# Optimization experiments

Measured on AMD Instinct MI355X. Metric: run time of the kernel, lower is better.

Reference implementation:

```python
import jax, jax.numpy as jnp
import numpy as np

V = 32000      # vocab_size
E = 256        # ModelConfig.n_embed
T_BLOCK = 2048 # ModelConfig.block_size
H = 4          # n_head (hardcoded in Bigram)
L = 3          # number of Blocks
HS = E // H    # head_size
EPS = 1e-5

def _ln(x, g, b):
    mu = jnp.mean(x, axis=-1, keepdims=True)
    var = jnp.var(x, axis=-1, keepdims=True)
    return (x - mu) * jax.lax.rsqrt(var + EPS) * g + b

def setup_inputs() -> dict:
    key = jax.random.key(0)
    ks = jax.random.split(key, 16)
    s = 0.02
    inp = {
        "idx": jax.random.randint(ks[0], (4, T_BLOCK), 0, V),
        "tok_emb": jax.random.normal(ks[1], (V, E), jnp.float32) * s,
        "pos_emb": jax.random.normal(ks[2], (T_BLOCK, E), jnp.float32) * s,
        # per-layer stacked params (heads concatenated -> full ExE projections)
        "Wq": jax.random.normal(ks[3], (L, E, E), jnp.float32) * s,
        "Wk": jax.random.normal(ks[4], (L, E, E), jnp.float32) * s,
        "Wv": jax.random.normal(ks[5], (L, E, E), jnp.float32) * s,
        "Wproj": jax.random.normal(ks[6], (L, E, E), jnp.float32) * s,
        "bproj": jnp.zeros((L, E), jnp.float32),
        "ln1_g": jnp.ones((L, E), jnp.float32),
        "ln1_b": jnp.zeros((L, E), jnp.float32),
        "W1": jax.random.normal(ks[7], (L, E, 4 * E), jnp.float32) * s,
        "b1": jnp.zeros((L, 4 * E), jnp.float32),
        "W2": jax.random.normal(ks[8], (L, 4 * E, E), jnp.float32) * s,
        "b2": jnp.zeros((L, E), jnp.float32),
        "ln2_g": jnp.ones((L, E), jnp.float32),
        "ln2_b": jnp.zeros((L, E), jnp.float32),
        "Wlm": jax.random.normal(ks[9], (E, V), jnp.float32) * s,
        "blm": jnp.zeros((V,), jnp.float32),
    }
    return inp

def reference(idx, tok_emb, pos_emb, Wq, Wk, Wv, Wproj, bproj, ln1_g, ln1_b,
              W1, b1, W2, b2, ln2_g, ln2_b, Wlm, blm):
    B, T = idx.shape
    x = tok_emb[idx] + pos_emb[:T]  # [B,T,E]
    causal = jnp.tril(jnp.ones((T, T), bool))
    # NOTE: source scales by C**0.5 with C = n_embed (not head_size)
    scale = 1.0 / jnp.sqrt(jnp.float32(E))
    for l in range(L):
        h = _ln(x, ln1_g[l], ln1_b[l])
        q = (h @ Wq[l]).reshape(B, T, H, HS).transpose(0, 2, 1, 3)
        k = (h @ Wk[l]).reshape(B, T, H, HS).transpose(0, 2, 1, 3)
        v = (h @ Wv[l]).reshape(B, T, H, HS).transpose(0, 2, 1, 3)
        wei = jnp.einsum('bhtd,bhsd->bhts', q, k) * scale
        wei = jnp.where(causal, wei, -jnp.inf)
        wei = jax.nn.softmax(wei, axis=-1)
        y = jnp.einsum('bhts,bhsd->bhtd', wei, v)
        y = y.transpose(0, 2, 1, 3).reshape(B, T, E)
        x = x + y @ Wproj[l] + bproj[l]
        h2 = _ln(x, ln2_g[l], ln2_b[l])
        x = x + jax.nn.relu(h2 @ W1[l] + b1[l]) @ W2[l] + b2[l]
    # ln_f exists in __init__ but is never applied in forward — skipped.
    logits = x @ Wlm + blm  # [B,T,V]
    return logits
```

## Files before the change

### kernel.cpp

```cpp
#include <hip/hip_runtime.h>
#include <hip/hip_bf16.h>

#define EMB 256
#define NHEAD 4
#define HSZ 64
#define NLAYER 3
#define TBLK 2048
#define VOCAB 32000
#define BATCH 4
#define LNEPS 1e-5f
#define BT (BATCH * TBLK)
#define QKVD (3 * EMB)

typedef __attribute__((ext_vector_type(8))) short bf16x8v;
typedef __attribute__((ext_vector_type(4))) float f32x4;
typedef unsigned short u16;
typedef unsigned int u32;

__device__ __forceinline__ u16 f2bf(float f) {
    union { float f; u32 u; } c; c.f = f;
    u32 r = c.u + 0x7fff + ((c.u >> 16) & 1);
    return (u16)(r >> 16);
}
__device__ __forceinline__ u32 pack2(float a, float b) {
    return (u32)f2bf(a) | ((u32)f2bf(b) << 16);
}

__device__ __forceinline__ void gload16(const u16* g, u16* l) {
    __builtin_amdgcn_global_load_lds(
        (__attribute__((address_space(1))) void*)g,
        (__attribute__((address_space(3))) void*)l, 16, 0, 0);
}

__global__ __launch_bounds__(256) void embed_kernel(
    const int* __restrict__ idx, const float* __restrict__ tok,
    const float* __restrict__ pos, float* __restrict__ x)
{
    const int row = blockIdx.x * 4 + (threadIdx.x >> 6);
    const int t = row & (TBLK - 1);
    const int token = idx[row];
    const int e = (threadIdx.x & 63) * 4;
    const float4 tv = *(const float4*)&tok[(size_t)token * EMB + e];
    const float4 pv = *(const float4*)&pos[(size_t)t * EMB + e];
    float4 o;
    o.x = tv.x + pv.x; o.y = tv.y + pv.y; o.z = tv.z + pv.z; o.w = tv.w + pv.w;
    *(float4*)&x[(size_t)row * EMB + e] = o;
}

__global__ __launch_bounds__(256) void ln_kernel(
    const float* __restrict__ x, const float* __restrict__ g,
    const float* __restrict__ b, u16* __restrict__ out)
{
    const int row = blockIdx.x * 4 + (threadIdx.x >> 6);
    const int e = (threadIdx.x & 63) * 4;
    const float4 xv = *(const float4*)&x[(size_t)row * EMB + e];
    float s1 = xv.x + xv.y + xv.z + xv.w;
    float s2 = xv.x * xv.x + xv.y * xv.y + xv.z * xv.z + xv.w * xv.w;
    #pragma unroll
    for (int off = 32; off >= 1; off >>= 1) {
        s1 += __shfl_xor(s1, off);
        s2 += __shfl_xor(s2, off);
    }
    const float mu  = s1 * (1.0f / EMB);
    const float var = s2 * (1.0f / EMB) - mu * mu;
    const float rs  = rsqrtf(var + LNEPS);
    const float4 gv = *(const float4*)&g[e];
    const float4 bv = *(const float4*)&b[e];
    ushort4 o;
    o.x = f2bf((xv.x - mu) * rs * gv.x + bv.x);
    o.y = f2bf((xv.y - mu) * rs * gv.y + bv.y);
    o.z = f2bf((xv.z - mu) * rs * gv.z + bv.z);
    o.w = f2bf((xv.w - mu) * rs * gv.w + bv.w);
    *(ushort4*)&out[(size_t)row * EMB + e] = o;
}

__global__ __launch_bounds__(256) void transpose_cast(
    const float* __restrict__ W, u16* __restrict__ Wt, int K, int N,
    size_t sW, size_t sWt)
{
    __shared__ float t[32][33];
    W  += (size_t)blockIdx.z * sW;
    Wt += (size_t)blockIdx.z * sWt;
    const int bx = blockIdx.x, by = blockIdx.y;
    const int tx = threadIdx.x, ty = threadIdx.y;
    #pragma unroll
    for (int i = 0; i < 32; i += 8)
        t[ty + i][tx] = W[(size_t)(by * 32 + ty + i) * N + bx * 32 + tx];
    __syncthreads();
    #pragma unroll
    for (int i = 0; i < 32; i += 8)
        Wt[(size_t)(bx * 32 + ty + i) * K + by * 32 + tx] = f2bf(t[tx][ty + i]);
}

__global__ __launch_bounds__(256) void transpose_qkvp(
    const float* __restrict__ Wq, const float* __restrict__ Wk,
    const float* __restrict__ Wv, const float* __restrict__ Wp,
    u16* __restrict__ Wqkvt, u16* __restrict__ Wprojt)
{
    __shared__ float t[32][33];
    const int which = blockIdx.z & 3, l = blockIdx.z >> 2;
    const float* W;
    u16* Wt;
    switch (which) {
        case 0: W = Wq + (size_t)l*EMB*EMB; Wt = Wqkvt + (size_t)l*QKVD*EMB;               break;
        case 1: W = Wk + (size_t)l*EMB*EMB; Wt = Wqkvt + (size_t)l*QKVD*EMB + EMB*EMB;     break;
        case 2: W = Wv + (size_t)l*EMB*EMB; Wt = Wqkvt + (size_t)l*QKVD*EMB + 2*EMB*EMB;   break;
        default:W = Wp + (size_t)l*EMB*EMB; Wt = Wprojt + (size_t)l*EMB*EMB;               break;
    }
    const int bx = blockIdx.x, by = blockIdx.y;
    const int tx = threadIdx.x, ty = threadIdx.y;
    #pragma unroll
    for (int i = 0; i < 32; i += 8)
        t[ty + i][tx] = W[(size_t)(by * 32 + ty + i) * EMB + bx * 32 + tx];
    __syncthreads();
    #pragma unroll
    for (int i = 0; i < 32; i += 8)
        Wt[(size_t)(bx * 32 + ty + i) * EMB + by * 32 + tx] = f2bf(t[tx][ty + i]);
}

template<int BNT, int BIAS, int RES, int RELU, int OUTBF>
__global__ __launch_bounds__(256) void mgemm(
    const u16* __restrict__ A, const u16* __restrict__ Bt,
    const float* __restrict__ bias, const float* __restrict__ res,
    void* __restrict__ Cv, int M, int N, int K)
{
    constexpr int MI = (BNT == 128) ? 4 : 2;
    __shared__ u16 Al[2][128 * 32];
    __shared__ u16 Bl[2][BNT * 32];
    const int tid = threadIdx.x;
    const int bm = blockIdx.x, bn = blockIdx.y;
    const int wid = tid >> 6, lane = tid & 63;
    const int wr = (BNT == 128) ? (wid >> 1) * 64 : wid * 32;
    const int wc = (BNT == 128) ? (wid & 1) * 64 : 0;
    const int fr = lane & 15, fq = lane >> 4;

    const int l4 = lane >> 2;
    const int lc_src = ((lane & 3) ^ ((l4 >> 1) & 3)) * 8;
    const u16* Aga = A  + (size_t)(bm * 128 + wid * 16 + l4) * K + lc_src;
    const u16* Bga = Bt + (size_t)(bn * BNT + wid * 16 + l4) * K + lc_src;
    const int lin = (wid * 16 + l4) * 32 + (lane & 3) * 8;

    const int rsw = (fq ^ ((fr >> 1) & 3)) * 8;

    f32x4 acc[MI][4];
    #pragma unroll
    for (int i = 0; i < MI; ++i)
        #pragma unroll
        for (int j = 0; j < 4; ++j)
            acc[i][j] = f32x4{0.f, 0.f, 0.f, 0.f};

    gload16(Aga,                  &Al[0][lin]);
    gload16(Aga + (size_t)64 * K, &Al[0][lin + 64 * 32]);
    gload16(Bga,                  &Bl[0][lin]);
    if (BNT == 128) gload16(Bga + (size_t)64 * K, &Bl[0][lin + 64 * 32]);

    int buf = 0;
    for (int k0 = 0; k0 < K; k0 += 32, buf ^= 1) {
        __syncthreads();
        if (k0 + 32 < K) {
            gload16(Aga + k0 + 32,                  &Al[buf ^ 1][lin]);
            gload16(Aga + (size_t)64 * K + k0 + 32, &Al[buf ^ 1][lin + 64 * 32]);
            gload16(Bga + k0 + 32,                  &Bl[buf ^ 1][lin]);
            if (BNT == 128)
                gload16(Bga + (size_t)64 * K + k0 + 32, &Bl[buf ^ 1][lin + 64 * 32]);
        }
        bf16x8v af[MI], bfr[4];
        #pragma unroll
        for (int mi = 0; mi < MI; ++mi)
            af[mi] = *(const bf16x8v*)&Al[buf][(wr + mi * 16 + fr) * 32 + rsw];
        #pragma unroll
        for (int ni = 0; ni < 4; ++ni)
            bfr[ni] = *(const bf16x8v*)&Bl[buf][(wc + ni * 16 + fr) * 32 + rsw];
        #pragma unroll
        for (int mi = 0; mi < MI; ++mi)
            #pragma unroll
            for (int ni = 0; ni < 4; ++ni)
                acc[mi][ni] = __builtin_amdgcn_mfma_f32_16x16x32_bf16(
                    af[mi], bfr[ni], acc[mi][ni], 0, 0, 0);
    }

    float* Cf = (float*)Cv;
    u16*   Cb = (u16*)Cv;
    #pragma unroll
    for (int mi = 0; mi < MI; ++mi) {
        #pragma unroll
        for (int j = 0; j < 4; ++j) {
            const int r = bm * 128 + wr + mi * 16 + fq * 4 + j;
            #pragma unroll
            for (int ni = 0; ni < 4; ++ni) {
                const int c = bn * BNT + wc + ni * 16 + fr;
                float v = acc[mi][ni][j];
                if (BIAS) v += bias[c];
                if (RELU) v = fmaxf(v, 0.f);
                if (RES)  v += res[(size_t)r * N + c];
                if (OUTBF) Cb[(size_t)r * N + c] = f2bf(v);
                else       Cf[(size_t)r * N + c] = v;
            }
        }
    }
}

__global__ __launch_bounds__(256) void attn_kernel(
    const u16* __restrict__ qkv, u16* __restrict__ y)
{
    constexpr int LDK = 72;
    __shared__ u16 Kl[2][64 * LDK];
    __shared__ u16 Vt[2][64 * LDK];

    const int tid = threadIdx.x;
    const int qt = (int)gridDim.x - 1 - (int)blockIdx.x;
    const int bh = blockIdx.y;
    const int b = bh >> 2, h = bh & 3;
    const int w = tid >> 6, lane = tid & 63;
    const int fr = lane & 15, fq = lane >> 4;
    const size_t rowbase = (size_t)b * TBLK;
    const int qoff = h * HSZ, koff = EMB + h * HSZ, voff = 2 * EMB + h * HSZ;
    const int qg = qt * 64 + w * 16 + fr;

    bf16x8v qf[2];
    #pragma unroll
    for (int ks = 0; ks < 2; ++ks)
        qf[ks] = *(const bf16x8v*)&qkv[(rowbase + qg) * QKVD + qoff + ks * 32 + fq * 8];

    f32x4 yac[4];
    #pragma unroll
    for (int mi = 0; mi < 4; ++mi) yac[mi] = f32x4{0.f, 0.f, 0.f, 0.f};
    float m = -1e30f, l = 0.f;

    const int skv = tid >> 2, sc = (tid & 3) * 16;
    const u16* kbase = &qkv[(rowbase + skv) * QKVD + koff + sc];
    const u16* vbase = &qkv[(rowbase + skv) * QKVD + voff + sc];

    bf16x8v kr0 = *(const bf16x8v*)kbase;
    bf16x8v kr1 = *(const bf16x8v*)(kbase + 8);
    bf16x8v vr0 = *(const bf16x8v*)vbase;
    bf16x8v vr1 = *(const bf16x8v*)(vbase + 8);

    int buf = 0;
    for (int kv0 = 0; kv0 <= qt * 64; kv0 += 64, buf ^= 1) {
        {
            u16* Kw = &Kl[buf][skv * LDK + sc];
            *(bf16x8v*)Kw = kr0; *(bf16x8v*)(Kw + 8) = kr1;
            #pragma unroll
            for (int i = 0; i < 8; ++i) Vt[buf][(sc + i) * LDK + skv] = (u16)vr0[i];
            #pragma unroll
            for (int i = 0; i < 8; ++i) Vt[buf][(sc + 8 + i) * LDK + skv] = (u16)vr1[i];
        }
        __syncthreads();
        if (kv0 + 64 <= qt * 64) {
            const size_t off = (size_t)(kv0 + 64) * QKVD;
            kr0 = *(const bf16x8v*)(kbase + off);
            kr1 = *(const bf16x8v*)(kbase + off + 8);
            vr0 = *(const bf16x8v*)(vbase + off);
            vr1 = *(const bf16x8v*)(vbase + off + 8);
        }

        f32x4 st[4];
        __builtin_amdgcn_s_setprio(1);
        #pragma unroll
        for (int mb = 0; mb < 4; ++mb) {
            st[mb] = f32x4{0.f, 0.f, 0.f, 0.f};
            #pragma unroll
            for (int ks = 0; ks < 2; ++ks) {
                const bf16x8v kf = *(const bf16x8v*)
                    &Kl[buf][(mb * 16 + fr) * LDK + ks * 32 + fq * 8];
                st[mb] = __builtin_amdgcn_mfma_f32_16x16x32_bf16(
                    kf, qf[ks], st[mb], 0, 0, 0);
            }
        }
        __builtin_amdgcn_s_setprio(0);
        float p[4][4];
        float mloc = -1e30f;
        #pragma unroll
        for (int mb = 0; mb < 4; ++mb)
            #pragma unroll
            for (int j = 0; j < 4; ++j) {
                const int kvg = kv0 + mb * 16 + fq * 4 + j;
                const float s = (kvg <= qg) ? st[mb][j] * 0.0625f : -1e30f;
                p[mb][j] = s;
                mloc = fmaxf(mloc, s);
            }
    mloc = fmaxf(mloc, __shfl_xor(mloc, 16));
        mloc = fmaxf(mloc, __shfl_xor(mloc, 32));
        const float mnew = fmaxf(m, mloc);
        const float alpha = __expf(m - mnew);
        float rsum = 0.f;
        #pragma unroll
        for (int mb = 0; mb < 4; ++mb)
            #pragma unroll
            for (int j = 0; j < 4; ++j) {
                p[mb][j] = __expf(p[mb][j] - mnew);
                rsum += p[mb][j];
            }
        rsum += __shfl_xor(rsum, 16);
        rsum += __shfl_xor(rsum, 32);
        l = l * alpha + rsum;
        m = mnew;
        #pragma unroll
        for (int mi = 0; mi < 4; ++mi) yac[mi] *= alpha;

        u32 pk[4][2];
        #pragma unroll
        for (int mb = 0; mb < 4; ++mb) {
            pk[mb][0] = pack2(p[mb][0], p[mb][1]);
            pk[mb][1] = pack2(p[mb][2], p[mb][3]);
        }
        #pragma unroll
        for (int ksv = 0; ksv < 2; ++ksv) {
            union { u32 u[4]; bf16x8v v; } pf;
            #pragma unroll
            for (int t = 0; t < 4; ++t) {
                const int srcl = ((fq & 1) * 2 + (t >> 1)) * 16 + fr;
                const u32 lo = __shfl(pk[ksv * 2 + 0][t & 1], srcl);
                const u32 hi = __shfl(pk[ksv * 2 + 1][t & 1], srcl);
                pf.u[t] = (fq >> 1) ? hi : lo;
            }
            __builtin_amdgcn_s_setprio(1);
            #pragma unroll
            for (int mi = 0; mi < 4; ++mi) {
                const bf16x8v vf = *(const bf16x8v*)
                    &Vt[buf][(mi * 16 + fr) * LDK + ksv * 32 + fq * 8];
                yac[mi] = __builtin_amdgcn_mfma_f32_16x16x32_bf16(
                    vf, pf.v, yac[mi], 0, 0, 0);
            }
            __builtin_amdgcn_s_setprio(0);
        }
    }

    const float inv = 1.f / l;
    #pragma unroll
    for (int mi = 0; mi < 4; ++mi) {
        ushort4 o;
        o.x = f2bf(yac[mi][0] * inv);
        o.y = f2bf(yac[mi][1] * inv);
        o.z = f2bf(yac[mi][2] * inv);
        o.w = f2bf(yac[mi][3] * inv);
        *(ushort4*)&y[(rowbase + qg) * EMB + h * HSZ + mi * 16 + fq * 4] = o;
    }
}

extern "C" void kernel_launch(void* const* d_in, const int* in_sizes, int n_in,
                              void* d_out, int out_size, void* d_ws, size_t ws_size,
                              hipStream_t stream) {
    const int*   idx   = (const int*)  d_in[0];
    const float* tok   = (const float*)d_in[1];
    const float* pos   = (const float*)d_in[2];
    const float* Wq    = (const float*)d_in[3];
    const float* Wk    = (const float*)d_in[4];
    const float* Wv    = (const float*)d_in[5];
    const float* Wproj = (const float*)d_in[6];
    const float* bproj = (const float*)d_in[7];
    const float* ln1g  = (const float*)d_in[8];
    const float* ln1b  = (const float*)d_in[9];
    const float* W1    = (const float*)d_in[10];
    const float* b1    = (const float*)d_in[11];
    const float* W2    = (const float*)d_in[12];
    const float* b2    = (const float*)d_in[13];
    const float* ln2g  = (const float*)d_in[14];
    const float* ln2b  = (const float*)d_in[15];
    const float* Wlm   = (const float*)d_in[16];
    const float* blm   = (const float*)d_in[17];
    float* out = (float*)d_out;

    float* x    = (float*)d_ws;
    u16*   hb   = (u16*)(x + (size_t)BT * EMB);
    u16*   qkvb = hb + (size_t)BT * EMB;
    u16*   yb   = qkvb + (size_t)BT * QKVD;
    u16*   hid  = qkvb;
    u16*   Wqkvt  = yb + (size_t)BT * EMB;
    u16*   Wprojt = Wqkvt  + (size_t)NLAYER * QKVD * EMB;
    u16*   W1t    = Wprojt + (size_t)NLAYER * EMB * EMB;
    u16*   W2t    = W1t    + (size_t)NLAYER * EMB * 4 * EMB;
    u16*   Wlmt   = W2t    + (size_t)NLAYER * 4 * EMB * EMB;

    const dim3 tb(32, 8);
    transpose_qkvp<<<dim3(8, 8, NLAYER * 4), tb, 0, stream>>>(
        Wq, Wk, Wv, Wproj, Wqkvt, Wprojt);
    transpose_cast<<<dim3(32, 8, NLAYER), tb, 0, stream>>>(
        W1, W1t, EMB, 4*EMB, (size_t)EMB*4*EMB, (size_t)EMB*4*EMB);
    transpose_cast<<<dim3(8, 32, NLAYER), tb, 0, stream>>>(
        W2, W2t, 4*EMB, EMB, (size_t)4*EMB*EMB, (size_t)4*EMB*EMB);
    transpose_cast<<<dim3(VOCAB/32, 8, 1), tb, 0, stream>>>(
        Wlm, Wlmt, EMB, VOCAB, 0, 0);

    embed_kernel<<<BT/4, 256, 0, stream>>>(idx, tok, pos, x);

    for (int l = 0; l < NLAYER; ++l) {
        ln_kernel<<<BT/4, 256, 0, stream>>>(x, ln1g + l*EMB, ln1b + l*EMB, hb);
        mgemm<128,0,0,0,1><<<dim3(BT/128, QKVD/128), 256, 0, stream>>>(
            hb, Wqkvt + (size_t)l*QKVD*EMB, nullptr, nullptr, qkvb, BT, QKVD, EMB);
        attn_kernel<<<dim3(TBLK/64, BATCH*NHEAD), 256, 0, stream>>>(qkvb, yb);
        mgemm<64,1,1,0,0><<<dim3(BT/128, EMB/64), 256, 0, stream>>>(
            yb, Wprojt + (size_t)l*EMB*EMB, bproj + l*EMB, x, x, BT, EMB, EMB);
        ln_kernel<<<BT/4, 256, 0, stream>>>(x, ln2g + l*EMB, ln2b + l*EMB, hb);
        mgemm<128,1,0,1,1><<<dim3(BT/128, 4*EMB/128), 256, 0, stream>>>(
            hb, W1t + (size_t)l*EMB*4*EMB, b1 + l*4*EMB, nullptr, hid, BT, 4*EMB, EMB);
        if (l < NLAYER - 1) {
            mgemm<64,1,1,0,0><<<dim3(BT/128, EMB/64), 256, 0, stream>>>(
                hid, W2t + (size_t)l*4*EMB*EMB, b2 + l*EMB, x, x, BT, EMB, 4*EMB);
        } else {
            mgemm<64,1,1,0,1><<<dim3(BT/128, EMB/64), 256, 0, stream>>>(
                hid, W2t + (size_t)l*4*EMB*EMB, b2 + l*EMB, x, hb, BT, EMB, 4*EMB);
        }
    }

    mgemm<128,1,0,0,0><<<dim3(BT/128, VOCAB/128), 256, 0, stream>>>(
        hb, Wlmt, blm, nullptr, out, BT, VOCAB, EMB);
}
```

Baseline: 690.2 us.

## Restructure GEMM to 64x64 tiles with full 256-wide K chunks in LDS

Replaces the double-buffered 128xBNT tile GEMM (K step 32) with a 64x64 tile that loads a whole 256-wide K chunk of A and B into LDS (64 KB) with an XOR swizzle, then runs 8 MFMA k-steps between barriers. This cuts the number of barriers and gives more blocks to fill the GPU, especially for the N=256 projections. The cost is lower arithmetic intensity per tile, no overlap of loads with compute, and heavy LDS use that limits occupancy. The large LM-head GEMM now launches 4x more blocks with smaller reuse.

```diff
diff --git a/kernel.cpp b/kernel.cpp
--- a/kernel.cpp
+++ b/kernel.cpp
@@ -118,77 +118,76 @@
         Wt[(size_t)(bx * 32 + ty + i) * EMB + by * 32 + tx] = f2bf(t[tx][ty + i]);
 }
 
-template<int BNT, int BIAS, int RES, int RELU, int OUTBF>
+template<int BIAS, int RES, int RELU, int OUTBF>
 __global__ __launch_bounds__(256) void mgemm(
     const u16* __restrict__ A, const u16* __restrict__ Bt,
     const float* __restrict__ bias, const float* __restrict__ res,
     void* __restrict__ Cv, int M, int N, int K)
 {
-    constexpr int MI = (BNT == 128) ? 4 : 2;
-    __shared__ u16 Al[2][128 * 32];
-    __shared__ u16 Bl[2][BNT * 32];
+    __shared__ u16 Al[64 * 256];
+    __shared__ u16 Bl[64 * 256];
     const int tid = threadIdx.x;
     const int bm = blockIdx.x, bn = blockIdx.y;
     const int wid = tid >> 6, lane = tid & 63;
-    const int wr = (BNT == 128) ? (wid >> 1) * 64 : wid * 32;
-    const int wc = (BNT == 128) ? (wid & 1) * 64 : 0;
+    const int wr = (wid >> 1) * 32, wc = (wid & 1) * 32;
     const int fr = lane & 15, fq = lane >> 4;
 
-    const int l4 = lane >> 2;
-    const int lc_src = ((lane & 3) ^ ((l4 >> 1) & 3)) * 8;
-    const u16* Aga = A  + (size_t)(bm * 128 + wid * 16 + l4) * K + lc_src;
-    const u16* Bga = Bt + (size_t)(bn * BNT + wid * 16 + l4) * K + lc_src;
-    const int lin = (wid * 16 + l4) * 32 + (lane & 3) * 8;
-
-    const int rsw = (fq ^ ((fr >> 1) & 3)) * 8;
-
-    f32x4 acc[MI][4];
-    #pragma unroll
-    for (int i = 0; i < MI; ++i)
-        #pragma unroll
-        for (int j = 0; j < 4; ++j)
+    const int srow = tid >> 5;
+    const int sch  = (tid & 31) ^ srow;
+    const u16* Ag = A  + (size_t)(bm * 64 + srow) * K + sch * 8;
+    const u16* Bg = Bt + (size_t)(bn * 64 + srow) * K + sch * 8;
+    const int ldst = tid * 8;
+
+    const int frs = fr & 7;
+
+    f32x4 acc[2][2];
+    #pragma unroll
+    for (int i = 0; i < 2; ++i)
+        #pragma unroll
+        for (int j = 0; j < 2; ++j)
             acc[i][j] = f32x4{0.f, 0.f, 0.f, 0.f};
 
-    gload16(Aga,                  &Al[0][lin]);
-    gload16(Aga + (size_t)64 * K, &Al[0][lin + 64 * 32]);
-    gload16(Bga,                  &Bl[0][lin]);
-    if (BNT == 128) gload16(Bga + (size_t)64 * K, &Bl[0][lin + 64 * 32]);
-
-    int buf = 0;
-    for (int k0 = 0; k0 < K; k0 += 32, buf ^= 1) {
+    const int nc = K >> 8;
+    for (int c = 0; c < nc; ++c) {
+        if (c) __syncthreads();
+        const size_t cofs = (size_t)c << 8;
+        #pragma unroll
+        for (int R = 0; R < 8; ++R)
+            gload16(Ag + cofs + (size_t)R * 8 * K, &Al[R * 2048 + ldst]);
+        #pragma unroll
+        for (int R = 0; R < 8; ++R)
+            gload16(Bg + cofs + (size_t)R * 8 * K, &Bl[R * 2048 + ldst]);
         __syncthreads();
-        if (k0 + 32 < K) {
-            gload16(Aga + k0 + 32,                  &Al[buf ^ 1][lin]);
-            gload16(Aga + (size_t)64 * K + k0 + 32, &Al[buf ^ 1][lin + 64 * 32]);
-            gload16(Bga + k0 + 32,                  &Bl[buf ^ 1][lin]);
-            if (BNT == 128)
-                gload16(Bga + (size_t)64 * K + k0 + 32, &Bl[buf ^ 1][lin + 64 * 32]);
-        }
-        bf16x8v af[MI], bfr[4];
-        #pragma unroll
-        for (int mi = 0; mi < MI; ++mi)
-            af[mi] = *(const bf16x8v*)&Al[buf][(wr + mi * 16 + fr) * 32 + rsw];
-        #pragma unroll
-        for (int ni = 0; ni < 4; ++ni)
-            bfr[ni] = *(const bf16x8v*)&Bl[buf][(wc + ni * 16 + fr) * 32 + rsw];
-        #pragma unroll
-        for (int mi = 0; mi < MI; ++mi)
-            #pragma unroll
-            for (int ni = 0; ni < 4; ++ni)
-                acc[mi][ni] = __builtin_amdgcn_mfma_f32_16x16x32_bf16(
-                    af[mi], bfr[ni], acc[mi][ni], 0, 0, 0);
+
+        #pragma unroll
+        for (int ks = 0; ks < 8; ++ks) {
+            const int s8 = (((ks * 4 + fq) ^ frs)) * 8;
+            bf16x8v af[2], bfv[2];
+            #pragma unroll
+            for (int mi = 0; mi < 2; ++mi)
+                af[mi] = *(const bf16x8v*)&Al[(wr + mi * 16 + fr) * 256 + s8];
+            #pragma unroll
+            for (int ni = 0; ni < 2; ++ni)
+                bfv[ni] = *(const bf16x8v*)&Bl[(wc + ni * 16 + fr) * 256 + s8];
+            #pragma unroll
+            for (int mi = 0; mi < 2; ++mi)
+                #pragma unroll
+                for (int ni = 0; ni < 2; ++ni)
+                    acc[mi][ni] = __builtin_amdgcn_mfma_f32_16x16x32_bf16(
+                        af[mi], bfv[ni], acc[mi][ni], 0, 0, 0);
+        }
     }
 
     float* Cf = (float*)Cv;
     u16*   Cb = (u16*)Cv;
     #pragma unroll
-    for (int mi = 0; mi < MI; ++mi) {
+    for (int mi = 0; mi < 2; ++mi) {
         #pragma unroll
         for (int j = 0; j < 4; ++j) {
-            const int r = bm * 128 + wr + mi * 16 + fq * 4 + j;
-            #pragma unroll
-            for (int ni = 0; ni < 4; ++ni) {
-                const int c = bn * BNT + wc + ni * 16 + fr;
+            const int r = bm * 64 + wr + mi * 16 + fq * 4 + j;
+            #pragma unroll
+            for (int ni = 0; ni < 2; ++ni) {
+                const int c = bn * 64 + wc + ni * 16 + fr;
                 float v = acc[mi][ni][j];
                 if (BIAS) v += bias[c];
                 if (RELU) v = fmaxf(v, 0.f);
@@ -280,7 +279,7 @@
                 p[mb][j] = s;
                 mloc = fmaxf(mloc, s);
             }
-    mloc = fmaxf(mloc, __shfl_xor(mloc, 16));
+        mloc = fmaxf(mloc, __shfl_xor(mloc, 16));
         mloc = fmaxf(mloc, __shfl_xor(mloc, 32));
         const float mnew = fmaxf(m, mloc);
         const float alpha = __expf(m - mnew);
@@ -387,23 +386,23 @@
 
     for (int l = 0; l < NLAYER; ++l) {
         ln_kernel<<<BT/4, 256, 0, stream>>>(x, ln1g + l*EMB, ln1b + l*EMB, hb);
-        mgemm<128,0,0,0,1><<<dim3(BT/128, QKVD/128), 256, 0, stream>>>(
+        mgemm<0,0,0,1><<<dim3(BT/64, QKVD/64), 256, 0, stream>>>(
             hb, Wqkvt + (size_t)l*QKVD*EMB, nullptr, nullptr, qkvb, BT, QKVD, EMB);
         attn_kernel<<<dim3(TBLK/64, BATCH*NHEAD), 256, 0, stream>>>(qkvb, yb);
-        mgemm<64,1,1,0,0><<<dim3(BT/128, EMB/64), 256, 0, stream>>>(
+        mgemm<1,1,0,0><<<dim3(BT/64, EMB/64), 256, 0, stream>>>(
             yb, Wprojt + (size_t)l*EMB*EMB, bproj + l*EMB, x, x, BT, EMB, EMB);
         ln_kernel<<<BT/4, 256, 0, stream>>>(x, ln2g + l*EMB, ln2b + l*EMB, hb);
-        mgemm<128,1,0,1,1><<<dim3(BT/128, 4*EMB/128), 256, 0, stream>>>(
+        mgemm<1,0,1,1><<<dim3(BT/64, 4*EMB/64), 256, 0, stream>>>(
             hb, W1t + (size_t)l*EMB*4*EMB, b1 + l*4*EMB, nullptr, hid, BT, 4*EMB, EMB);
         if (l < NLAYER - 1) {
-            mgemm<64,1,1,0,0><<<dim3(BT/128, EMB/64), 256, 0, stream>>>(
+            mgemm<1,1,0,0><<<dim3(BT/64, EMB/64), 256, 0, stream>>>(
                 hid, W2t + (size_t)l*4*EMB*EMB, b2 + l*EMB, x, x, BT, EMB, 4*EMB);
         } else {
-            mgemm<64,1,1,0,1><<<dim3(BT/128, EMB/64), 256, 0, stream>>>(
+            mgemm<1,1,0,1><<<dim3(BT/64, EMB/64), 256, 0, stream>>>(
                 hid, W2t + (size_t)l*4*EMB*EMB, b2 + l*EMB, x, hb, BT, EMB, 4*EMB);
         }
     }
 
-    mgemm<128,1,0,0,0><<<dim3(BT/128, VOCAB/128), 256, 0, stream>>>(
+    mgemm<1,0,0,0><<<dim3(BT/64, VOCAB/64), 256, 0, stream>>>(
         hb, Wlmt, blm, nullptr, out, BT, VOCAB, EMB);
 }
```

Measured after the change: 776.0 us. 1.12x slower.

## Fuse LayerNorm into residual GEMM epilogues and embedding kernel

Applied to the files above, without the earlier changes.

Adds a GEMM kernel whose block covers 32 full rows of all 256 output columns. It applies bias and the residual add, then computes the following LayerNorm in the epilogue through a cross-wave shared-memory reduction. Embedding is fused with the first LN, which removes the separate LN launches and their extra read of x. The new GEMM loads through registers rather than async LDS loads and uses a smaller M tile with the full B matrix in each block, so per-block B traffic and the occupancy balance change.

```diff
diff --git a/kernel.cpp b/kernel.cpp
--- a/kernel.cpp
+++ b/kernel.cpp
@@ -32,9 +32,10 @@
         (__attribute__((address_space(3))) void*)l, 16, 0, 0);
 }
 
-__global__ __launch_bounds__(256) void embed_kernel(
+__global__ __launch_bounds__(256) void embed_ln_kernel(
     const int* __restrict__ idx, const float* __restrict__ tok,
-    const float* __restrict__ pos, float* __restrict__ x)
+    const float* __restrict__ pos, const float* __restrict__ g,
+    const float* __restrict__ b, float* __restrict__ x, u16* __restrict__ hb)
 {
     const int row = blockIdx.x * 4 + (threadIdx.x >> 6);
     const int t = row & (TBLK - 1);
@@ -42,18 +43,10 @@
     const int e = (threadIdx.x & 63) * 4;
     const float4 tv = *(const float4*)&tok[(size_t)token * EMB + e];
     const float4 pv = *(const float4*)&pos[(size_t)t * EMB + e];
-    float4 o;
-    o.x = tv.x + pv.x; o.y = tv.y + pv.y; o.z = tv.z + pv.z; o.w = tv.w + pv.w;
-    *(float4*)&x[(size_t)row * EMB + e] = o;
-}
-
-__global__ __launch_bounds__(256) void ln_kernel(
-    const float* __restrict__ x, const float* __restrict__ g,
-    const float* __restrict__ b, u16* __restrict__ out)
-{
-    const int row = blockIdx.x * 4 + (threadIdx.x >> 6);
-    const int e = (threadIdx.x & 63) * 4;
-    const float4 xv = *(const float4*)&x[(size_t)row * EMB + e];
+    float4 xv;
+    xv.x = tv.x + pv.x; xv.y = tv.y + pv.y; xv.z = tv.z + pv.z; xv.w = tv.w + pv.w;
+    *(float4*)&x[(size_t)row * EMB + e] = xv;
+
     float s1 = xv.x + xv.y + xv.z + xv.w;
     float s2 = xv.x * xv.x + xv.y * xv.y + xv.z * xv.z + xv.w * xv.w;
     #pragma unroll
@@ -71,7 +64,7 @@
     o.y = f2bf((xv.y - mu) * rs * gv.y + bv.y);
     o.z = f2bf((xv.z - mu) * rs * gv.z + bv.z);
     o.w = f2bf((xv.w - mu) * rs * gv.w + bv.w);
-    *(ushort4*)&out[(size_t)row * EMB + e] = o;
+    *(ushort4*)&hb[(size_t)row * EMB + e] = o;
 }
 
 __global__ __launch_bounds__(256) void transpose_cast(
@@ -118,33 +111,32 @@
         Wt[(size_t)(bx * 32 + ty + i) * EMB + by * 32 + tx] = f2bf(t[tx][ty + i]);
 }
 
-template<int BNT, int BIAS, int RES, int RELU, int OUTBF>
+template<int BIAS, int RES, int RELU, int OUTBF>
 __global__ __launch_bounds__(256) void mgemm(
     const u16* __restrict__ A, const u16* __restrict__ Bt,
     const float* __restrict__ bias, const float* __restrict__ res,
     void* __restrict__ Cv, int M, int N, int K)
 {
-    constexpr int MI = (BNT == 128) ? 4 : 2;
     __shared__ u16 Al[2][128 * 32];
-    __shared__ u16 Bl[2][BNT * 32];
+    __shared__ u16 Bl[2][128 * 32];
     const int tid = threadIdx.x;
     const int bm = blockIdx.x, bn = blockIdx.y;
     const int wid = tid >> 6, lane = tid & 63;
-    const int wr = (BNT == 128) ? (wid >> 1) * 64 : wid * 32;
-    const int wc = (BNT == 128) ? (wid & 1) * 64 : 0;
+    const int wr = (wid >> 1) * 64;
+    const int wc = (wid & 1) * 64;
     const int fr = lane & 15, fq = lane >> 4;
 
     const int l4 = lane >> 2;
     const int lc_src = ((lane & 3) ^ ((l4 >> 1) & 3)) * 8;
     const u16* Aga = A  + (size_t)(bm * 128 + wid * 16 + l4) * K + lc_src;
-    const u16* Bga = Bt + (size_t)(bn * BNT + wid * 16 + l4) * K + lc_src;
+    const u16* Bga = Bt + (size_t)(bn * 128 + wid * 16 + l4) * K + lc_src;
     const int lin = (wid * 16 + l4) * 32 + (lane & 3) * 8;
 
     const int rsw = (fq ^ ((fr >> 1) & 3)) * 8;
 
-    f32x4 acc[MI][4];
-    #pragma unroll
-    for (int i = 0; i < MI; ++i)
+    f32x4 acc[4][4];
+    #pragma unroll
+    for (int i = 0; i < 4; ++i)
         #pragma unroll
         for (int j = 0; j < 4; ++j)
             acc[i][j] = f32x4{0.f, 0.f, 0.f, 0.f};
@@ -152,7 +144,7 @@
     gload16(Aga,                  &Al[0][lin]);
     gload16(Aga + (size_t)64 * K, &Al[0][lin + 64 * 32]);
     gload16(Bga,                  &Bl[0][lin]);
-    if (BNT == 128) gload16(Bga + (size_t)64 * K, &Bl[0][lin + 64 * 32]);
+    gload16(Bga + (size_t)64 * K, &Bl[0][lin + 64 * 32]);
 
     int buf = 0;
     for (int k0 = 0; k0 < K; k0 += 32, buf ^= 1) {
@@ -161,18 +153,17 @@
             gload16(Aga + k0 + 32,                  &Al[buf ^ 1][lin]);
             gload16(Aga + (size_t)64 * K + k0 + 32, &Al[buf ^ 1][lin + 64 * 32]);
             gload16(Bga + k0 + 32,                  &Bl[buf ^ 1][lin]);
-            if (BNT == 128)
-                gload16(Bga + (size_t)64 * K + k0 + 32, &Bl[buf ^ 1][lin + 64 * 32]);
-        }
-        bf16x8v af[MI], bfr[4];
-        #pragma unroll
-        for (int mi = 0; mi < MI; ++mi)
+            gload16(Bga + (size_t)64 * K + k0 + 32, &Bl[buf ^ 1][lin + 64 * 32]);
+        }
+        bf16x8v af[4], bfr[4];
+        #pragma unroll
+        for (int mi = 0; mi < 4; ++mi)
             af[mi] = *(const bf16x8v*)&Al[buf][(wr + mi * 16 + fr) * 32 + rsw];
         #pragma unroll
         for (int ni = 0; ni < 4; ++ni)
             bfr[ni] = *(const bf16x8v*)&Bl[buf][(wc + ni * 16 + fr) * 32 + rsw];
         #pragma unroll
-        for (int mi = 0; mi < MI; ++mi)
+        for (int mi = 0; mi < 4; ++mi)
             #pragma unroll
             for (int ni = 0; ni < 4; ++ni)
                 acc[mi][ni] = __builtin_amdgcn_mfma_f32_16x16x32_bf16(
@@ -182,19 +173,135 @@
     float* Cf = (float*)Cv;
     u16*   Cb = (u16*)Cv;
     #pragma unroll
-    for (int mi = 0; mi < MI; ++mi) {
+    for (int mi = 0; mi < 4; ++mi) {
         #pragma unroll
         for (int j = 0; j < 4; ++j) {
             const int r = bm * 128 + wr + mi * 16 + fq * 4 + j;
             #pragma unroll
             for (int ni = 0; ni < 4; ++ni) {
-                const int c = bn * BNT + wc + ni * 16 + fr;
+                const int c = bn * 128 + wc + ni * 16 + fr;
                 float v = acc[mi][ni][j];
                 if (BIAS) v += bias[c];
                 if (RELU) v = fmaxf(v, 0.f);
                 if (RES)  v += res[(size_t)r * N + c];
                 if (OUTBF) Cb[(size_t)r * N + c] = f2bf(v);
                 else       Cf[(size_t)r * N + c] = v;
+            }
+        }
+    }
+}
+
+template<int LN>
+__global__ __launch_bounds__(256) void mgemm_ln(
+    const u16* __restrict__ A, const u16* __restrict__ Bt,
+    const float* __restrict__ bias, float* __restrict__ x,
+    const float* __restrict__ g, const float* __restrict__ b,
+    u16* __restrict__ hb, int K)
+{
+    constexpr int LDW = 34;
+    __shared__ u16 Al[2][32 * LDW];
+    __shared__ u16 Bl[2][256 * LDW];
+    __shared__ float part[4][32][2];
+
+    const int tid = threadIdx.x;
+    const int bm = blockIdx.x;
+    const int w = tid >> 6, lane = tid & 63;
+    const int fr = lane & 15, fq = lane >> 4;
+
+    const int ar = tid >> 2, ak = (tid & 3) * 8;
+    const u16* Ag = A + (size_t)(bm * 32 + ar) * K + ak;
+    const u16* Bg = Bt + (size_t)tid * K;
+
+    bf16x8v apre;
+    bf16x8v bpre[4];
+    if (tid < 128) apre = *(const bf16x8v*)Ag;
+    #pragma unroll
+    for (int c = 0; c < 4; ++c) bpre[c] = *(const bf16x8v*)(Bg + c * 8);
+
+    f32x4 acc[2][4];
+    #pragma unroll
+    for (int i = 0; i < 2; ++i)
+        #pragma unroll
+        for (int j = 0; j < 4; ++j)
+            acc[i][j] = f32x4{0.f, 0.f, 0.f, 0.f};
+
+    int buf = 0;
+    for (int k0 = 0; k0 < K; k0 += 32, buf ^= 1) {
+        if (tid < 128) *(bf16x8v*)&Al[buf][ar * LDW + ak] = apre;
+        #pragma unroll
+        for (int c = 0; c < 4; ++c)
+            *(bf16x8v*)&Bl[buf][tid * LDW + c * 8] = bpre[c];
+        __syncthreads();
+        if (k0 + 32 < K) {
+            if (tid < 128) apre = *(const bf16x8v*)(Ag + k0 + 32);
+            #pragma unroll
+            for (int c = 0; c < 4; ++c)
+                bpre[c] = *(const bf16x8v*)(Bg + k0 + 32 + c * 8);
+        }
+        bf16x8v af[2], bfv[4];
+        #pragma unroll
+        for (int mi = 0; mi < 2; ++mi)
+            af[mi] = *(const bf16x8v*)&Al[buf][(mi * 16 + fr) * LDW + fq * 8];
+        #pragma unroll
+        for (int ni = 0; ni < 4; ++ni)
+            bfv[ni] = *(const bf16x8v*)&Bl[buf][(w * 64 + ni * 16 + fr) * LDW + fq * 8];
+        #pragma unroll
+        for (int mi = 0; mi < 2; ++mi)
+            #pragma unroll
+            for (int ni = 0; ni < 4; ++ni)
+                acc[mi][ni] = __builtin_amdgcn_mfma_f32_16x16x32_bf16(
+                    af[mi], bfv[ni], acc[mi][ni], 0, 0, 0);
+    }
+
+    float vv[2][4][4];
+    #pragma unroll
+    for (int mi = 0; mi < 2; ++mi) {
+        #pragma unroll
+        for (int j = 0; j < 4; ++j) {
+            const int rloc = mi * 16 + fq * 4 + j;
+            const size_t r = (size_t)(bm * 32 + rloc);
+            float s1 = 0.f, s2 = 0.f;
+            #pragma unroll
+            for (int ni = 0; ni < 4; ++ni) {
+                const int c = w * 64 + ni * 16 + fr;
+                float v = acc[mi][ni][j] + bias[c] + x[r * EMB + c];
+                vv[mi][ni][j] = v;
+                if (LN) {
+                    x[r * EMB + c] = v;
+                    s1 += v; s2 += v * v;
+                } else {
+                    hb[r * EMB + c] = f2bf(v);
+                }
+            }
+            if (LN) {
+                #pragma unroll
+                for (int off = 8; off >= 1; off >>= 1) {
+                    s1 += __shfl_xor(s1, off);
+                    s2 += __shfl_xor(s2, off);
+                }
+                if (fr == 0) { part[w][rloc][0] = s1; part[w][rloc][1] = s2; }
+            }
+        }
+    }
+    if (!LN) return;
+    __syncthreads();
+    #pragma unroll
+    for (int mi = 0; mi < 2; ++mi) {
+        #pragma unroll
+        for (int j = 0; j < 4; ++j) {
+            const int rloc = mi * 16 + fq * 4 + j;
+            const size_t r = (size_t)(bm * 32 + rloc);
+            const float t1 = part[0][rloc][0] + part[1][rloc][0]
+                           + part[2][rloc][0] + part[3][rloc][0];
+            const float t2 = part[0][rloc][1] + part[1][rloc][1]
+                           + part[2][rloc][1] + part[3][rloc][1];
+            const float mu  = t1 * (1.0f / EMB);
+            const float var = t2 * (1.0f / EMB) - mu * mu;
+            const float rsd = rsqrtf(var + LNEPS);
+            #pragma unroll
+            for (int ni = 0; ni < 4; ++ni) {
+                const int c = w * 64 + ni * 16 + fr;
+                hb[r * EMB + c] = f2bf((vv[mi][ni][j] - mu) * rsd * g[c] + b[c]);
             }
         }
     }
@@ -280,7 +387,7 @@
                 p[mb][j] = s;
                 mloc = fmaxf(mloc, s);
             }
-    mloc = fmaxf(mloc, __shfl_xor(mloc, 16));
+        mloc = fmaxf(mloc, __shfl_xor(mloc, 16));
         mloc = fmaxf(mloc, __shfl_xor(mloc, 32));
         const float mnew = fmaxf(m, mloc);
         const float alpha = __expf(m - mnew);
@@ -383,27 +490,28 @@
     transpose_cast<<<dim3(VOCAB/32, 8, 1), tb, 0, stream>>>(
         Wlm, Wlmt, EMB, VOCAB, 0, 0);
 
-    embed_kernel<<<BT/4, 256, 0, stream>>>(idx, tok, pos, x);
+    embed_ln_kernel<<<BT/4, 256, 0, stream>>>(idx, tok, pos, ln1g, ln1b, x, hb);
 
     for (int l = 0; l < NLAYER; ++l) {
-        ln_kernel<<<BT/4, 256, 0, stream>>>(x, ln1g + l*EMB, ln1b + l*EMB, hb);
-        mgemm<128,0,0,0,1><<<dim3(BT/128, QKVD/128), 256, 0, stream>>>(
+        mgemm<0,0,0,1><<<dim3(BT/128, QKVD/128), 256, 0, stream>>>(
             hb, Wqkvt + (size_t)l*QKVD*EMB, nullptr, nullptr, qkvb, BT, QKVD, EMB);
         attn_kernel<<<dim3(TBLK/64, BATCH*NHEAD), 256, 0, stream>>>(qkvb, yb);
-        mgemm<64,1,1,0,0><<<dim3(BT/128, EMB/64), 256, 0, stream>>>(
-            yb, Wprojt + (size_t)l*EMB*EMB, bproj + l*EMB, x, x, BT, EMB, EMB);
-        ln_kernel<<<BT/4, 256, 0, stream>>>(x, ln2g + l*EMB, ln2b + l*EMB, hb);
-        mgemm<128,1,0,1,1><<<dim3(BT/128, 4*EMB/128), 256, 0, stream>>>(
+        mgemm_ln<1><<<BT/32, 256, 0, stream>>>(
+            yb, Wprojt + (size_t)l*EMB*EMB, bproj + l*EMB, x,
+            ln2g + l*EMB, ln2b + l*EMB, hb, EMB);
+        mgemm<1,0,1,1><<<dim3(BT/128, 4*EMB/128), 256, 0, stream>>>(
             hb, W1t + (size_t)l*EMB*4*EMB, b1 + l*4*EMB, nullptr, hid, BT, 4*EMB, EMB);
         if (l < NLAYER - 1) {
-            mgemm<64,1,1,0,0><<<dim3(BT/128, EMB/64), 256, 0, stream>>>(
-                hid, W2t + (size_t)l*4*EMB*EMB, b2 + l*EMB, x, x, BT, EMB, 4*EMB);
+            mgemm_ln<1><<<BT/32, 256, 0, stream>>>(
+                hid, W2t + (size_t)l*4*EMB*EMB, b2 + l*EMB, x,
+                ln1g + (l+1)*EMB, ln1b + (l+1)*EMB, hb, 4*EMB);
         } else {
-            mgemm<64,1,1,0,1><<<dim3(BT/128, EMB/64), 256, 0, stream>>>(
-                hid, W2t + (size_t)l*4*EMB*EMB, b2 + l*EMB, x, hb, BT, EMB, 4*EMB);
-        }
-    }
-
-    mgemm<128,1,0,0,0><<<dim3(BT/128, VOCAB/128), 256, 0, stream>>>(
+            mgemm_ln<0><<<BT/32, 256, 0, stream>>>(
+                hid, W2t + (size_t)l*4*EMB*EMB, b2 + l*EMB, x,
+                nullptr, nullptr, hb, 4*EMB);
+        }
+    }
+
+    mgemm<1,0,0,0><<<dim3(BT/128, VOCAB/128), 256, 0, stream>>>(
         hb, Wlmt, blm, nullptr, out, BT, VOCAB, EMB);
 }
```

Measured after the change: 744.7 us. +7.9%, slower.

## Add K=256 GEMM with resident A tile and fuse embed with first layernorm

Applied to the files above, without the earlier changes.

Adds a specialized GEMM for K=256 that loads the whole 64x256 A tile into LDS once and streams B through a 4-stage ring with explicit vmcnt waits. It is used for the QKV, proj, W1 and the large LM-head GEMM. It also fuses the embedding with the first layernorm, saving one launch and one pass over x. The smaller 64-row M tiles double the grid size and change the reuse balance. The LM-head GEMM dominates, and its epilogue still uses scalar fp32 stores.

```diff
diff --git a/kernel.cpp b/kernel.cpp
--- a/kernel.cpp
+++ b/kernel.cpp
@@ -32,9 +32,16 @@
         (__attribute__((address_space(3))) void*)l, 16, 0, 0);
 }
 
-__global__ __launch_bounds__(256) void embed_kernel(
+__device__ __forceinline__ void waitcnt_vm(int n) {
+    if (n == 0)      asm volatile("s_waitcnt vmcnt(0)" ::: "memory");
+    else if (n == 2) asm volatile("s_waitcnt vmcnt(2)" ::: "memory");
+    else             asm volatile("s_waitcnt vmcnt(4)" ::: "memory");
+}
+
+__global__ __launch_bounds__(256) void embed_ln_kernel(
     const int* __restrict__ idx, const float* __restrict__ tok,
-    const float* __restrict__ pos, float* __restrict__ x)
+    const float* __restrict__ pos, const float* __restrict__ g,
+    const float* __restrict__ b, float* __restrict__ x, u16* __restrict__ hb)
 {
     const int row = blockIdx.x * 4 + (threadIdx.x >> 6);
     const int t = row & (TBLK - 1);
@@ -42,9 +49,28 @@
     const int e = (threadIdx.x & 63) * 4;
     const float4 tv = *(const float4*)&tok[(size_t)token * EMB + e];
     const float4 pv = *(const float4*)&pos[(size_t)t * EMB + e];
-    float4 o;
-    o.x = tv.x + pv.x; o.y = tv.y + pv.y; o.z = tv.z + pv.z; o.w = tv.w + pv.w;
-    *(float4*)&x[(size_t)row * EMB + e] = o;
+    float4 xv;
+    xv.x = tv.x + pv.x; xv.y = tv.y + pv.y; xv.z = tv.z + pv.z; xv.w = tv.w + pv.w;
+    *(float4*)&x[(size_t)row * EMB + e] = xv;
+
+    float s1 = xv.x + xv.y + xv.z + xv.w;
+    float s2 = xv.x * xv.x + xv.y * xv.y + xv.z * xv.z + xv.w * xv.w;
+    #pragma unroll
+    for (int off = 32; off >= 1; off >>= 1) {
+        s1 += __shfl_xor(s1, off);
+        s2 += __shfl_xor(s2, off);
+    }
+    const float mu  = s1 * (1.0f / EMB);
+    const float var = s2 * (1.0f / EMB) - mu * mu;
+    const float rs  = rsqrtf(var + LNEPS);
+    const float4 gv = *(const float4*)&g[e];
+    const float4 bv = *(const float4*)&b[e];
+    ushort4 o;
+    o.x = f2bf((xv.x - mu) * rs * gv.x + bv.x);
+    o.y = f2bf((xv.y - mu) * rs * gv.y + bv.y);
+    o.z = f2bf((xv.z - mu) * rs * gv.z + bv.z);
+    o.w = f2bf((xv.w - mu) * rs * gv.w + bv.w);
+    *(ushort4*)&hb[(size_t)row * EMB + e] = o;
 }
 
 __global__ __launch_bounds__(256) void ln_kernel(
@@ -118,6 +144,98 @@
         Wt[(size_t)(bx * 32 + ty + i) * EMB + by * 32 + tx] = f2bf(t[tx][ty + i]);
 }
 
+template<int BIAS, int RES, int RELU, int OUTBF>
+__global__ __launch_bounds__(256) void mgemm_k256(
+    const u16* __restrict__ A, const u16* __restrict__ Bt,
+    const float* __restrict__ bias, const float* __restrict__ res,
+    void* __restrict__ Cv, int N)
+{
+    __shared__ u16 Al[64 * 256];
+    __shared__ u16 Bl[4][128 * 32];
+    const int tid = threadIdx.x;
+    const int bm = blockIdx.x, bn = blockIdx.y;
+    const int wid = tid >> 6, lane = tid & 63;
+    const int wr = (wid >> 1) * 32, wc = (wid & 1) * 64;
+    const int fr = lane & 15, fq = lane >> 4;
+
+    {
+        const int arow = tid >> 5;
+        const int achk = tid & 31;
+        const u16* Asrc = A + (size_t)(bm * 64 + arow) * 256 + ((achk ^ arow) * 8);
+        u16* Adst = &Al[arow * 256 + achk * 8];
+        #pragma unroll
+        for (int R = 0; R < 8; ++R)
+            gload16(Asrc + (size_t)R * 8 * 256, Adst + R * 8 * 256);
+    }
+    const int l4 = lane >> 2;
+    const int lc_src = ((lane & 3) ^ ((l4 >> 1) & 3)) * 8;
+    const u16* Bga = Bt + (size_t)(bn * 128 + wid * 16 + l4) * 256 + lc_src;
+    const int blin = (wid * 16 + l4) * 32 + (lane & 3) * 8;
+
+    #pragma unroll
+    for (int p = 0; p < 3; ++p) {
+        gload16(Bga + p * 32,                    &Bl[p][blin]);
+        gload16(Bga + (size_t)64 * 256 + p * 32, &Bl[p][blin + 64 * 32]);
+    }
+
+    const int rswB = (fq ^ ((fr >> 1) & 3)) * 8;
+    const int frs = fr & 7;
+
+    f32x4 acc[2][4];
+    #pragma unroll
+    for (int i = 0; i < 2; ++i)
+        #pragma unroll
+        for (int j = 0; j < 4; ++j)
+            acc[i][j] = f32x4{0.f, 0.f, 0.f, 0.f};
+
+    #pragma unroll
+    for (int ks = 0; ks < 8; ++ks) {
+        waitcnt_vm(ks <= 5 ? 4 : (ks == 6 ? 2 : 0));
+        asm volatile("s_waitcnt lgkmcnt(0)" ::: "memory");
+        asm volatile("s_barrier" ::: "memory");
+        __builtin_amdgcn_sched_barrier(0);
+        if (ks <= 4) {
+            gload16(Bga + (ks + 3) * 32,                    &Bl[(ks + 3) & 3][blin]);
+            gload16(Bga + (size_t)64 * 256 + (ks + 3) * 32, &Bl[(ks + 3) & 3][blin + 64 * 32]);
+        }
+        bf16x8v af[2], bfr[4];
+        #pragma unroll
+        for (int mi = 0; mi < 2; ++mi) {
+            const int row = wr + mi * 16 + fr;
+            af[mi] = *(const bf16x8v*)&Al[row * 256 + (((ks * 4 + fq) ^ frs) * 8)];
+        }
+        #pragma unroll
+        for (int ni = 0; ni < 4; ++ni)
+            bfr[ni] = *(const bf16x8v*)&Bl[ks & 3][(wc + ni * 16 + fr) * 32 + rswB];
+        #pragma unroll
+        for (int mi = 0; mi < 2; ++mi)
+            #pragma unroll
+            for (int ni = 0; ni < 4; ++ni)
+                acc[mi][ni] = __builtin_amdgcn_mfma_f32_16x16x32_bf16(
+                    af[mi], bfr[ni], acc[mi][ni], 0, 0, 0);
+    }
+
+    float* Cf = (float*)Cv;
+    u16*   Cb = (u16*)Cv;
+    #pragma unroll
+    for (int mi = 0; mi < 2; ++mi) {
+        #pragma unroll
+        for (int j = 0; j < 4; ++j) {
+            const int r = bm * 64 + wr + mi * 16 + fq * 4 + j;
+            #pragma unroll
+            for (int ni = 0; ni < 4; ++ni) {
+                const int c = bn * 128 + wc + ni * 16 + fr;
+                float v = acc[mi][ni][j];
+                if (BIAS) v += bias[c];
+                if (RELU) v = fmaxf(v, 0.f);
+                if (RES)  v += res[(size_t)r * N + c];
+                if (OUTBF) Cb[(size_t)r * N + c] = f2bf(v);
+                else       Cf[(size_t)r * N + c] = v;
+            }
+        }
+    }
+}
+
 template<int BNT, int BIAS, int RES, int RELU, int OUTBF>
 __global__ __launch_bounds__(256) void mgemm(
     const u16* __restrict__ A, const u16* __restrict__ Bt,
@@ -280,7 +398,7 @@
                 p[mb][j] = s;
                 mloc = fmaxf(mloc, s);
             }
-    mloc = fmaxf(mloc, __shfl_xor(mloc, 16));
+        mloc = fmaxf(mloc, __shfl_xor(mloc, 16));
         mloc = fmaxf(mloc, __shfl_xor(mloc, 32));
         const float mnew = fmaxf(m, mloc);
         const float alpha = __expf(m - mnew);
@@ -383,27 +501,28 @@
     transpose_cast<<<dim3(VOCAB/32, 8, 1), tb, 0, stream>>>(
         Wlm, Wlmt, EMB, VOCAB, 0, 0);
 
-    embed_kernel<<<BT/4, 256, 0, stream>>>(idx, tok, pos, x);
+    embed_ln_kernel<<<BT/4, 256, 0, stream>>>(idx, tok, pos, ln1g, ln1b, x, hb);
 
     for (int l = 0; l < NLAYER; ++l) {
-        ln_kernel<<<BT/4, 256, 0, stream>>>(x, ln1g + l*EMB, ln1b + l*EMB, hb);
-        mgemm<128,0,0,0,1><<<dim3(BT/128, QKVD/128), 256, 0, stream>>>(
-            hb, Wqkvt + (size_t)l*QKVD*EMB, nullptr, nullptr, qkvb, BT, QKVD, EMB);
+        mgemm_k256<0,0,0,1><<<dim3(BT/64, QKVD/128), 256, 0, stream>>>(
+            hb, Wqkvt + (size_t)l*QKVD*EMB, nullptr, nullptr, qkvb, QKVD);
         attn_kernel<<<dim3(TBLK/64, BATCH*NHEAD), 256, 0, stream>>>(qkvb, yb);
-        mgemm<64,1,1,0,0><<<dim3(BT/128, EMB/64), 256, 0, stream>>>(
-            yb, Wprojt + (size_t)l*EMB*EMB, bproj + l*EMB, x, x, BT, EMB, EMB);
+        mgemm_k256<1,1,0,0><<<dim3(BT/64, EMB/128), 256, 0, stream>>>(
+            yb, Wprojt + (size_t)l*EMB*EMB, bproj + l*EMB, x, x, EMB);
         ln_kernel<<<BT/4, 256, 0, stream>>>(x, ln2g + l*EMB, ln2b + l*EMB, hb);
-        mgemm<128,1,0,1,1><<<dim3(BT/128, 4*EMB/128), 256, 0, stream>>>(
-            hb, W1t + (size_t)l*EMB*4*EMB, b1 + l*4*EMB, nullptr, hid, BT, 4*EMB, EMB);
+        mgemm_k256<1,0,1,1><<<dim3(BT/64, 4*EMB/128), 256, 0, stream>>>(
+            hb, W1t + (size_t)l*EMB*4*EMB, b1 + l*4*EMB, nullptr, hid, 4*EMB);
         if (l < NLAYER - 1) {
             mgemm<64,1,1,0,0><<<dim3(BT/128, EMB/64), 256, 0, stream>>>(
                 hid, W2t + (size_t)l*4*EMB*EMB, b2 + l*EMB, x, x, BT, EMB, 4*EMB);
+            ln_kernel<<<BT/4, 256, 0, stream>>>(
+                x, ln1g + (l+1)*EMB, ln1b + (l+1)*EMB, hb);
         } else {
             mgemm<64,1,1,0,1><<<dim3(BT/128, EMB/64), 256, 0, stream>>>(
                 hid, W2t + (size_t)l*4*EMB*EMB, b2 + l*EMB, x, hb, BT, EMB, 4*EMB);
         }
     }
 
-    mgemm<128,1,0,0,0><<<dim3(BT/128, VOCAB/128), 256, 0, stream>>>(
-        hb, Wlmt, blm, nullptr, out, BT, VOCAB, EMB);
-}
+    mgemm_k256<1,0,0,0><<<dim3(BT/64, VOCAB/128), 256, 0, stream>>>(
+        hb, Wlmt, blm, nullptr, out, VOCAB);
+}
```

Result: slower. 786.8 us (+14.0%).
